# Kernel tuning notes

Measured on AMD Instinct MI355X. Metric: run time of the kernel, lower is better.

The kernel has to match this reference:

```python
import jax, jax.numpy as jnp
import numpy as np

FOCUS_RADIUS = 20.0
FOCUS_WEIGHT = 10.0
SPREAD_PENALTY = 1.0
EPS = 1e-8


def setup_inputs() -> dict:
    key = jax.random.key(0)
    k1, k2 = jax.random.split(key)
    B, WL, H, W = 16, 8, 512, 512
    predictions = jax.random.uniform(k1, (B, WL, H, W), dtype=jnp.float32)
    targets = jax.random.uniform(k2, (B, WL, H, W), dtype=jnp.float32)
    return {"predictions": predictions, "targets": targets}


def reference(predictions, targets):
    B, WL, H, W = predictions.shape
    dt = predictions.dtype
    ys = jnp.arange(H, dtype=dt)[:, None]   # [H,1]
    xs = jnp.arange(W, dtype=dt)[None, :]   # [1,W]

    # base MSE loss
    base_loss = jnp.mean((predictions - targets) ** 2)

    # target energy centroids (detached in the original via .item())
    tsum = targets.sum((-2, -1))                      # [B,WL]
    valid = tsum >= EPS                               # center exists
    ts_safe = jnp.where(valid, tsum, 1.0)
    cy = jax.lax.stop_gradient((targets * ys).sum((-2, -1)) / ts_safe)  # [B,WL]
    cx = jax.lax.stop_gradient((targets * xs).sum((-2, -1)) / ts_safe)  # [B,WL]

    # squared distance to target center, per image  [B,WL,H,W]
    dist_sq = (ys - cy[..., None, None]) ** 2 + (xs - cx[..., None, None]) ** 2
    focus_mask = (dist_sq <= FOCUS_RADIUS * FOCUS_RADIUS).astype(dt)

    pred_total = predictions.sum((-2, -1))            # [B,WL]
    focus_energy = (predictions * focus_mask).sum((-2, -1))
    spread = (predictions * dist_sq).sum((-2, -1))
    pt_safe = jnp.where(pred_total > EPS, pred_total, 1.0)

    active = valid & (pred_total > EPS)
    focus_loss = jnp.sum(jnp.where(active, (1.0 - focus_energy / pt_safe) ** 2, 0.0))
    spread_loss = jnp.sum(jnp.where(active, spread / pt_safe, 0.0))

    return base_loss + FOCUS_WEIGHT * focus_loss + SPREAD_PENALTY * spread_loss
```

## Files before the change

kernel.cpp:

```cpp
#include <hip/hip_runtime.h>


#define HH 512
#define WW 512
#define IMG_PIX (HH * WW)
#define VEC_PER_IMG (IMG_PIX / 4)
#define BLOCKS_PER_IMG 8
#define VPB (VEC_PER_IMG / BLOCKS_PER_IMG)
#define THREADS 256
#define TILE_V 512
#define NT (VPB / TILE_V)
#define EPSF 1e-8f
#define R2 400.0f

typedef float f4 __attribute__((ext_vector_type(4)));

__device__ __forceinline__ float wave_reduce_sum(float v) {
    v += __shfl_down(v, 32);
    v += __shfl_down(v, 16);
    v += __shfl_down(v, 8);
    v += __shfl_down(v, 4);
    v += __shfl_down(v, 2);
    v += __shfl_down(v, 1);
    return v;
}

__device__ __forceinline__ double wave_reduce_sum_d(double v) {
    v += __shfl_down(v, 32);
    v += __shfl_down(v, 16);
    v += __shfl_down(v, 8);
    v += __shfl_down(v, 4);
    v += __shfl_down(v, 2);
    v += __shfl_down(v, 1);
    return v;
}

__device__ __forceinline__ void gl16(const f4* g, f4* l) {
    __builtin_amdgcn_global_load_lds(
        (const __attribute__((address_space(1))) void*)g,
        (__attribute__((address_space(3))) void*)l, 16, 0, 0);
}

__global__ void __launch_bounds__(THREADS) stream_kernel(
        const f4* __restrict__ pred, const f4* __restrict__ tgt,
        float* __restrict__ part) {
    __shared__ f4 bufT[2][TILE_V];
    __shared__ f4 bufP[2][TILE_V];

    const int tid  = threadIdx.x;
    const int w    = tid >> 6, lane = tid & 63;
    const int blk  = blockIdx.x;
    const int sub  = blk & (BLOCKS_PER_IMG - 1);
    const int gb0  = blk * VPB;
    const int ivb  = sub * VPB;
    const int o0   = w * 128, o1 = o0 + 64;

    float ts = 0.f, ty = 0.f, tx = 0.f, mse = 0.f;
    float m0 = 0.f, my = 0.f, mx = 0.f, m2 = 0.f;

    gl16(&tgt [gb0 + o0 + lane], &bufT[0][o0]);
    gl16(&tgt [gb0 + o1 + lane], &bufT[0][o1]);
    gl16(&pred[gb0 + o0 + lane], &bufP[0][o0]);
    gl16(&pred[gb0 + o1 + lane], &bufP[0][o1]);

    for (int t = 0; t < NT; ++t) {
        asm volatile("s_waitcnt lgkmcnt(0)" ::: "memory");
        __builtin_amdgcn_s_barrier();
        __builtin_amdgcn_sched_barrier(0);
        if (t + 1 < NT) {
            const int d  = (t + 1) & 1;
            const int gb = gb0 + (t + 1) * TILE_V;
            gl16(&tgt [gb + o0 + lane], &bufT[d][o0]);
            gl16(&tgt [gb + o1 + lane], &bufT[d][o1]);
            gl16(&pred[gb + o0 + lane], &bufP[d][o0]);
            gl16(&pred[gb + o1 + lane], &bufP[d][o1]);
            asm volatile("s_waitcnt vmcnt(4)" ::: "memory");
        } else {
            asm volatile("s_waitcnt vmcnt(0)" ::: "memory");
        }
        __builtin_amdgcn_s_barrier();
        __builtin_amdgcn_sched_barrier(0);

        const int d = t & 1;
#pragma unroll
        for (int u = 0; u < TILE_V / THREADS; ++u) {
            const int pos = u * THREADS + tid;
            const f4 tv = bufT[d][pos];
            const f4 pv = bufP[d][pos];
            const int iv = ivb + t * TILE_V + pos;
            const float y  = (float)(iv >> 7);
            const float x0 = (float)((iv & 127) << 2);

            const float tsum = tv[0] + tv[1] + tv[2] + tv[3];
            const float tw1  = tv[1] + 2.f * tv[2] + 3.f * tv[3];
            ts += tsum;
            ty += y * tsum;
            tx += x0 * tsum + tw1;

            const float d0 = pv[0] - tv[0], d1 = pv[1] - tv[1],
                        d2 = pv[2] - tv[2], d3 = pv[3] - tv[3];
            mse += d0 * d0 + d1 * d1 + d2 * d2 + d3 * d3;

            const float psum = pv[0] + pv[1] + pv[2] + pv[3];
            const float pw1  = pv[1] + 2.f * pv[2] + 3.f * pv[3];
            const float pw2  = pv[1] + 4.f * pv[2] + 9.f * pv[3];
            m0 += psum;
            my += y * psum;
            mx += x0 * psum + pw1;
            m2 += (y * y + x0 * x0) * psum + 2.f * x0 * pw1 + pw2;
        }
    }

    float vals[8] = {ts, ty, tx, mse, m0, my, mx, m2};
    __shared__ float red[4][8];
#pragma unroll
    for (int k = 0; k < 8; ++k) vals[k] = wave_reduce_sum(vals[k]);
    if (lane == 0)
#pragma unroll
        for (int k = 0; k < 8; ++k) red[w][k] = vals[k];
    __syncthreads();
    if (tid < 8)
        part[blk * 8 + tid] = red[0][tid] + red[1][tid] + red[2][tid] + red[3][tid];
}

__global__ void __launch_bounds__(THREADS) focus_kernel(
        const float* __restrict__ pred, const float* __restrict__ part,
        double* __restrict__ vout, double* __restrict__ mout) {
    const int img = blockIdx.x;
    const int tid = threadIdx.x;
    __shared__ float mom[8];
    {
        float v[8] = {0.f, 0.f, 0.f, 0.f, 0.f, 0.f, 0.f, 0.f};
        if (tid < BLOCKS_PER_IMG) {
            const float* p = part + (img * BLOCKS_PER_IMG + tid) * 8;
#pragma unroll
            for (int k = 0; k < 8; ++k) v[k] = p[k];
        }
        if (tid < 64) {
#pragma unroll
            for (int k = 0; k < 8; ++k) v[k] = wave_reduce_sum(v[k]);
            if (tid == 0)
#pragma unroll
                for (int k = 0; k < 8; ++k) mom[k] = v[k];
        }
    }
    __syncthreads();

    const float ts = mom[0];
    float fe = 0.f;
    if (ts >= EPSF) {
        const float cy = mom[1] / ts;
        const float cx = mom[2] / ts;
        const int ylo = max(0, (int)ceilf(cy - 20.f) - 1);
        const int yhi = min(HH - 1, (int)floorf(cy + 20.f) + 1);
        const int xlo = max(0, (int)ceilf(cx - 20.f) - 1);
        const int xhi = min(WW - 1, (int)floorf(cx + 20.f) + 1);
        const float* p = pred + (size_t)img * IMG_PIX;
        const int wv = tid >> 6;
        const int xx = xlo + (tid & 63);
        if (xx <= xhi) {
            const float dx = (float)xx - cx;
            const float dx2 = dx * dx;
            for (int y = ylo + wv; y <= yhi; y += 4) {
                const float dy = (float)y - cy;
                if (dy * dy + dx2 <= R2) fe += p[(y << 9) + xx];
            }
        }
    }
    __shared__ float redf[4];
    fe = wave_reduce_sum(fe);
    if ((tid & 63) == 0) redf[tid >> 6] = fe;
    __syncthreads();
    if (tid == 0) {
        const float fet = redf[0] + redf[1] + redf[2] + redf[3];
        const float m0 = mom[4];
        double v = 0.0;
        if (ts >= EPSF && m0 > EPSF) {
            const double dcy = (double)mom[1] / (double)ts;
            const double dcx = (double)mom[2] / (double)ts;
            const double spread = (double)mom[7] - 2.0 * dcy * (double)mom[5]
                                - 2.0 * dcx * (double)mom[6]
                                + (dcy * dcy + dcx * dcx) * (double)m0;
            const double r = 1.0 - (double)fet / (double)m0;
            v = 10.0 * r * r + spread / (double)m0;
        }
        vout[img] = v;
        mout[img] = (double)mom[3];
    }
}

__global__ void __launch_bounds__(128) final_kernel(
        const double* __restrict__ vout, const double* __restrict__ mout,
        float* __restrict__ out, int nimg, double inv_n) {
    const int i = threadIdx.x;
    double v = 0.0, m = 0.0;
    if (i < nimg) { v = vout[i]; m = mout[i]; }
    __shared__ double redv[2], redm[2];
    v = wave_reduce_sum_d(v);
    m = wave_reduce_sum_d(m);
    if ((i & 63) == 0) { redv[i >> 6] = v; redm[i >> 6] = m; }
    __syncthreads();
    if (i == 0)
        out[0] = (float)((redm[0] + redm[1]) * inv_n + redv[0] + redv[1]);
}

extern "C" void kernel_launch(void* const* d_in, const int* in_sizes, int n_in,
                              void* d_out, int out_size, void* d_ws, size_t ws_size,
                              hipStream_t stream) {
    const float* pred = (const float*)d_in[0];
    const float* tgt  = (const float*)d_in[1];
    float* out = (float*)d_out;

    const int n = in_sizes[0];
    const int nimg = n / IMG_PIX;
    const int nblk = nimg * BLOCKS_PER_IMG;

    float*  part = (float*)d_ws;
    double* vout = (double*)((char*)d_ws + 32768);
    double* mout = vout + nimg;

    stream_kernel<<<nblk, THREADS, 0, stream>>>(
        (const f4*)pred, (const f4*)tgt, part);
    focus_kernel<<<nimg, THREADS, 0, stream>>>(pred, part, vout, mout);
    final_kernel<<<1, 128, 0, stream>>>(vout, mout, out, nimg, 1.0 / (double)n);
}
```

Baseline: 51.95 us.

## Fuse stream, focus and final kernels via last-block atomic counters

Merges the three kernel launches into one. The last block to finish for each image, detected with an atomic counter and threadfences, runs the focus-window sum and the per-image loss. The last image to finish then does the global reduction. This removes two launch gaps and their tail idle time, but adds a hipMemsetAsync to reset the counters and hardcodes the image count to 128.

```diff
diff --git a/kernel.cpp b/kernel.cpp
--- a/kernel.cpp
+++ b/kernel.cpp
@@ -9,7 +9,8 @@
 #define VPB (VEC_PER_IMG / BLOCKS_PER_IMG)
 #define THREADS 256
 #define TILE_V 512
-#define NT (VPB / TILE_V)
+#define NTILE (VPB / TILE_V)
+#define NIMG 128
 #define EPSF 1e-8f
 #define R2 400.0f
 
@@ -41,15 +42,18 @@
         (__attribute__((address_space(3))) void*)l, 16, 0, 0);
 }
 
-__global__ void __launch_bounds__(THREADS) stream_kernel(
+__global__ void __launch_bounds__(THREADS) fused_kernel(
         const f4* __restrict__ pred, const f4* __restrict__ tgt,
-        float* __restrict__ part) {
+        float* __restrict__ part, unsigned* __restrict__ cnt,
+        double* __restrict__ vout, double* __restrict__ mout,
+        float* __restrict__ out, double inv_n) {
     __shared__ f4 bufT[2][TILE_V];
     __shared__ f4 bufP[2][TILE_V];
 
     const int tid  = threadIdx.x;
     const int w    = tid >> 6, lane = tid & 63;
     const int blk  = blockIdx.x;
+    const int img  = blk / BLOCKS_PER_IMG;
     const int sub  = blk & (BLOCKS_PER_IMG - 1);
     const int gb0  = blk * VPB;
     const int ivb  = sub * VPB;
@@ -63,11 +67,11 @@
     gl16(&pred[gb0 + o0 + lane], &bufP[0][o0]);
     gl16(&pred[gb0 + o1 + lane], &bufP[0][o1]);
 
-    for (int t = 0; t < NT; ++t) {
+    for (int t = 0; t < NTILE; ++t) {
         asm volatile("s_waitcnt lgkmcnt(0)" ::: "memory");
         __builtin_amdgcn_s_barrier();
         __builtin_amdgcn_sched_barrier(0);
-        if (t + 1 < NT) {
+        if (t + 1 < NTILE) {
             const int d  = (t + 1) & 1;
             const int gb = gb0 + (t + 1) * TILE_V;
             gl16(&tgt [gb + o0 + lane], &bufT[d][o0]);
@@ -119,15 +123,19 @@
 #pragma unroll
         for (int k = 0; k < 8; ++k) red[w][k] = vals[k];
     __syncthreads();
-    if (tid < 8)
+    if (tid < 8) {
         part[blk * 8 + tid] = red[0][tid] + red[1][tid] + red[2][tid] + red[3][tid];
-}
-
-__global__ void __launch_bounds__(THREADS) focus_kernel(
-        const float* __restrict__ pred, const float* __restrict__ part,
-        double* __restrict__ vout, double* __restrict__ mout) {
-    const int img = blockIdx.x;
-    const int tid = threadIdx.x;
+        __threadfence();
+    }
+    __syncthreads();
+
+    __shared__ bool amLast;
+    if (tid == 0)
+        amLast = (atomicAdd(&cnt[img], 1u) == BLOCKS_PER_IMG - 1);
+    __syncthreads();
+    if (!amLast) return;
+    __threadfence();
+
     __shared__ float mom[8];
     {
         float v[8] = {0.f, 0.f, 0.f, 0.f, 0.f, 0.f, 0.f, 0.f};
@@ -146,16 +154,16 @@
     }
     __syncthreads();
 
-    const float ts = mom[0];
+    const float tsum = mom[0];
     float fe = 0.f;
-    if (ts >= EPSF) {
-        const float cy = mom[1] / ts;
-        const float cx = mom[2] / ts;
+    if (tsum >= EPSF) {
+        const float cy = mom[1] / tsum;
+        const float cx = mom[2] / tsum;
         const int ylo = max(0, (int)ceilf(cy - 20.f) - 1);
         const int yhi = min(HH - 1, (int)floorf(cy + 20.f) + 1);
         const int xlo = max(0, (int)ceilf(cx - 20.f) - 1);
         const int xhi = min(WW - 1, (int)floorf(cx + 20.f) + 1);
-        const float* p = pred + (size_t)img * IMG_PIX;
+        const float* p = (const float*)pred + (size_t)img * IMG_PIX;
         const int wv = tid >> 6;
         const int xx = xlo + (tid & 63);
         if (xx <= xhi) {
@@ -171,37 +179,37 @@
     fe = wave_reduce_sum(fe);
     if ((tid & 63) == 0) redf[tid >> 6] = fe;
     __syncthreads();
+
+    __shared__ bool amFinal;
     if (tid == 0) {
         const float fet = redf[0] + redf[1] + redf[2] + redf[3];
-        const float m0 = mom[4];
+        const float pm0 = mom[4];
         double v = 0.0;
-        if (ts >= EPSF && m0 > EPSF) {
-            const double dcy = (double)mom[1] / (double)ts;
-            const double dcx = (double)mom[2] / (double)ts;
+        if (tsum >= EPSF && pm0 > EPSF) {
+            const double dcy = (double)mom[1] / (double)tsum;
+            const double dcx = (double)mom[2] / (double)tsum;
             const double spread = (double)mom[7] - 2.0 * dcy * (double)mom[5]
                                 - 2.0 * dcx * (double)mom[6]
-                                + (dcy * dcy + dcx * dcx) * (double)m0;
-            const double r = 1.0 - (double)fet / (double)m0;
-            v = 10.0 * r * r + spread / (double)m0;
+                                + (dcy * dcy + dcx * dcx) * (double)pm0;
+            const double r = 1.0 - (double)fet / (double)pm0;
+            v = 10.0 * r * r + spread / (double)pm0;
         }
         vout[img] = v;
         mout[img] = (double)mom[3];
-    }
-}
-
-__global__ void __launch_bounds__(128) final_kernel(
-        const double* __restrict__ vout, const double* __restrict__ mout,
-        float* __restrict__ out, int nimg, double inv_n) {
-    const int i = threadIdx.x;
-    double v = 0.0, m = 0.0;
-    if (i < nimg) { v = vout[i]; m = mout[i]; }
-    __shared__ double redv[2], redm[2];
-    v = wave_reduce_sum_d(v);
-    m = wave_reduce_sum_d(m);
-    if ((i & 63) == 0) { redv[i >> 6] = v; redm[i >> 6] = m; }
-    __syncthreads();
-    if (i == 0)
-        out[0] = (float)((redm[0] + redm[1]) * inv_n + redv[0] + redv[1]);
+        __threadfence();
+        amFinal = (atomicAdd(&cnt[NIMG], 1u) == NIMG - 1);
+    }
+    __syncthreads();
+    if (!amFinal) return;
+    __threadfence();
+
+    if (tid < 64) {
+        double v = vout[tid] + vout[tid + 64];
+        double m = mout[tid] + mout[tid + 64];
+        v = wave_reduce_sum_d(v);
+        m = wave_reduce_sum_d(m);
+        if (tid == 0) out[0] = (float)(m * inv_n + v);
+    }
 }
 
 extern "C" void kernel_launch(void* const* d_in, const int* in_sizes, int n_in,
@@ -212,15 +220,15 @@
     float* out = (float*)d_out;
 
     const int n = in_sizes[0];
-    const int nimg = n / IMG_PIX;
-    const int nblk = nimg * BLOCKS_PER_IMG;
-
-    float*  part = (float*)d_ws;
-    double* vout = (double*)((char*)d_ws + 32768);
-    double* mout = vout + nimg;
-
-    stream_kernel<<<nblk, THREADS, 0, stream>>>(
-        (const f4*)pred, (const f4*)tgt, part);
-    focus_kernel<<<nimg, THREADS, 0, stream>>>(pred, part, vout, mout);
-    final_kernel<<<1, 128, 0, stream>>>(vout, mout, out, nimg, 1.0 / (double)n);
-}
+    const int nblk = NIMG * BLOCKS_PER_IMG;
+
+    float*    part = (float*)d_ws;
+    unsigned* cnt  = (unsigned*)((char*)d_ws + 32768);
+    double*   vout = (double*)((char*)d_ws + 34816);
+    double*   mout = vout + NIMG;
+
+    hipMemsetAsync(cnt, 0, (NIMG + 1) * sizeof(unsigned), stream);
+    fused_kernel<<<nblk, THREADS, 0, stream>>>(
+        (const f4*)pred, (const f4*)tgt, part, cnt, vout, mout, out,
+        1.0 / (double)n);
+}
```

Result: slower. 117.9 us (+126.9%).
